# Performance work log

Measured on AMD Instinct MI355X. Metric: run time of the kernel, lower is better.

The kernel has to match this reference:

```python
import jax, jax.numpy as jnp
import numpy as np

B, S, D, H = 2, 2048, 1024, 16
HD = D // H  # 64

def _make_freqs():
    # flux-style rotation matrices: [1,1,S,HD//2,2,2]
    theta = 10000.0
    inv = 1.0 / (theta ** (np.arange(0, HD, 2, dtype=np.float32) / HD))  # [HD//2]
    pos = np.arange(S, dtype=np.float32)
    ang = pos[:, None] * inv[None, :]  # [S, HD//2]
    cos, sin = np.cos(ang), np.sin(ang)
    rot = np.stack([np.stack([cos, -sin], -1), np.stack([sin, cos], -1)], -2)  # [S,HD//2,2,2]
    return jnp.asarray(rot[None, None], dtype=jnp.float32)

def setup_inputs() -> dict:
    key = jax.random.key(0)
    ks = jax.random.split(key, 9)
    sc = 1.0 / np.sqrt(D)
    return {
        "x": jax.random.normal(ks[0], (B, S, D), jnp.float32),
        "freqs": _make_freqs(),
        "Wq": jax.random.normal(ks[1], (D, D), jnp.float32) * sc,
        "bq": jax.random.normal(ks[2], (D,), jnp.float32) * 0.01,
        "Wk": jax.random.normal(ks[3], (D, D), jnp.float32) * sc,
        "bk": jax.random.normal(ks[4], (D,), jnp.float32) * 0.01,
        "Wv": jax.random.normal(ks[5], (D, D), jnp.float32) * sc,
        "bv": jax.random.normal(ks[6], (D,), jnp.float32) * 0.01,
        "Wo": jax.random.normal(ks[7], (D, D), jnp.float32) * sc,
        "bo": jax.random.normal(ks[8], (D,), jnp.float32) * 0.01,
    }

def _apply_rope(xq, xk, freqs):
    # xq/xk: [B,H,S,HD]; freqs: [1,1,S,HD//2,2,2]
    def rot(t):
        t_ = t.reshape(*t.shape[:-1], -1, 1, 2)  # [B,H,S,HD//2,1,2]
        out = freqs[..., 0] * t_[..., 0] + freqs[..., 1] * t_[..., 1]  # [B,H,S,HD//2,2]
        return out.reshape(t.shape).astype(t.dtype)
    return rot(xq), rot(xk)

def reference(x, freqs, Wq, bq, Wk, bk, Wv, bv, Wo, bo):
    b, s, _ = x.shape
    # QKV projections (torch Linear: x @ W.T + b)
    q = (x @ Wq.T + bq).reshape(b, s, H, HD).transpose(0, 2, 1, 3)  # [B,H,S,HD]
    k = (x @ Wk.T + bk).reshape(b, s, H, HD).transpose(0, 2, 1, 3)
    v = (x @ Wv.T + bv).reshape(b, s, H, HD).transpose(0, 2, 1, 3)
    q, k = _apply_rope(q, k, freqs)
    # scaled dot product attention, no mask, no dropout
    scale = 1.0 / jnp.sqrt(jnp.asarray(HD, x.dtype))
    scores = jnp.einsum("bhqd,bhkd->bhqk", q, k) * scale
    attn = jax.nn.softmax(scores, axis=-1)
    o = jnp.einsum("bhqk,bhkd->bhqd", attn, v)  # [B,H,S,HD]
    o = o.transpose(0, 2, 1, 3).reshape(b, s, D)
    return o @ Wo.T + bo
```

## Files before the change

kernel.cpp:

```cpp
#include <hip/hip_runtime.h>
#include <cmath>

#define B_ 2
#define S_ 2048
#define D_ 1024
#define H_ 16
#define HD_ 64
#define M_ 4096

typedef __attribute__((ext_vector_type(8))) short short8;
typedef __attribute__((ext_vector_type(4))) short short4v;
typedef __attribute__((ext_vector_type(4))) float f32x4;

__device__ __forceinline__ short f2bf(float x) {
    unsigned u = __builtin_bit_cast(unsigned, x);
    u += 0x7fffu + ((u >> 16) & 1u);
    return (short)(u >> 16);
}

__device__ __forceinline__ void gload_lds16(const short* g, short* l) {
    __builtin_amdgcn_global_load_lds(
        (const __attribute__((address_space(1))) unsigned int*)g,
        (__attribute__((address_space(3))) unsigned int*)l, 16, 0, 0);
}

__global__ __launch_bounds__(256) void cast_all_kernel(
    const float* __restrict__ x,  const float* __restrict__ Wq,
    const float* __restrict__ Wk, const float* __restrict__ Wv,
    const float* __restrict__ Wo,
    short* __restrict__ xb, short* __restrict__ Wqkvb, short* __restrict__ Wob)
{
    const size_t i = (size_t)blockIdx.x * 256 + threadIdx.x;
    const float* src; short* dst; size_t off;
    if (i < 1048576)      { src = x;  dst = xb;              off = i; }
    else if (i < 1310720) { src = Wq; dst = Wqkvb;           off = i - 1048576; }
    else if (i < 1572864) { src = Wk; dst = Wqkvb + 1048576; off = i - 1310720; }
    else if (i < 1835008) { src = Wv; dst = Wqkvb + 2097152; off = i - 1572864; }
    else                  { src = Wo; dst = Wob;             off = i - 1835008; }
    float4 v = ((const float4*)src)[off];
    short4v o = { f2bf(v.x), f2bf(v.y), f2bf(v.z), f2bf(v.w) };
    ((short4v*)dst)[off] = o;
}

template<int MODE, int TM, int TN>
__global__ __launch_bounds__(256) void gemm_chunk(
    const short* __restrict__ A, const short* __restrict__ Bw,
    const float* __restrict__ b0p, const float* __restrict__ b1p, const float* __restrict__ b2p,
    const float* __restrict__ freqs,
    void* __restrict__ out0, void* __restrict__ out1, void* __restrict__ out2)
{
    constexpr int RT = TM / 32, CT = TN / 32;
    __shared__ __align__(16) short As[4*TM*32];
    __shared__ __align__(16) short Bs[4*TN*32];
    const int t = threadIdx.x;
    const int w = t >> 6;
    const int lane = t & 63;
    const int qd = lane >> 4, l = lane & 15;
    const int n0 = blockIdx.x * TN, m0 = blockIdx.y * TM;
    const int wr = (w >> 1) * (TM/2), wc = (w & 1) * (TN/2);
    const int srow = lane >> 2;
    const int scol = (lane & 3) * 8;

    f32x4 acc[RT][CT] = {};

    for (int k0 = 0; k0 < 1024; k0 += 128) {
        __syncthreads();
        #pragma unroll
        for (int sub = 0; sub < 4; ++sub) {
            #pragma unroll
            for (int j = 0; j < TM/64; ++j) {
                const int rr = (j*4 + w) * 16;
                gload_lds16(A + (size_t)(m0 + rr + srow)*1024 + k0 + sub*32 + scol,
                            &As[sub*TM*32 + rr*32]);
            }
            #pragma unroll
            for (int j = 0; j < TN/64; ++j) {
                const int rr = (j*4 + w) * 16;
                gload_lds16(Bw + (size_t)(n0 + rr + srow)*1024 + k0 + sub*32 + scol,
                            &Bs[sub*TN*32 + rr*32]);
            }
        }
        __syncthreads();
        #pragma unroll
        for (int sub = 0; sub < 4; ++sub) {
            short8 af[RT], bf[CT];
            #pragma unroll
            for (int rt = 0; rt < RT; ++rt)
                af[rt] = *(const short8*)&As[sub*TM*32 + (wr + rt*16 + l)*32 + qd*8];
            #pragma unroll
            for (int ct = 0; ct < CT; ++ct)
                bf[ct] = *(const short8*)&Bs[sub*TN*32 + (wc + ct*16 + l)*32 + qd*8];
            #pragma unroll
            for (int rt = 0; rt < RT; ++rt)
                #pragma unroll
                for (int ct = 0; ct < CT; ++ct)
                    acc[rt][ct] = __builtin_amdgcn_mfma_f32_16x16x32_bf16(af[rt], bf[ct], acc[rt][ct], 0, 0, 0);
        }
    }

    if (MODE == 0) {
        float* out = (float*)out0;
        #pragma unroll
        for (int rt = 0; rt < RT; ++rt)
            #pragma unroll
            for (int ct = 0; ct < CT; ++ct) {
                const int n = n0 + wc + ct*16 + l;
                const float bias = b0p[n];
                #pragma unroll
                for (int r = 0; r < 4; ++r) {
                    const int m = m0 + wr + rt*16 + qd*4 + r;
                    out[(size_t)m*1024 + n] = acc[rt][ct][r] + bias;
                }
            }
    } else {
        const int sel = n0 >> 10;
        const int nb = n0 & 1023;
        const float* bias = (sel == 0) ? b0p : (sel == 1) ? b1p : b2p;
        if (sel < 2) {
            short* outg = (short*)((sel == 0) ? out0 : out1);
            #pragma unroll
            for (int rt = 0; rt < RT; ++rt)
                #pragma unroll
                for (int ct = 0; ct < CT; ++ct) {
                    const int d = nb + wc + ct*16 + l;
                    const float bsv = bias[d];
                    const int h = d >> 6, hd = d & 63;
                    #pragma unroll
                    for (int r = 0; r < 4; ++r) {
                        const int m = m0 + wr + rt*16 + qd*4 + r;
                        const int bb = m >> 11, s = m & 2047;
                        float val = acc[rt][ct][r] + bsv;
                        float pv = __shfl_xor(val, 1);
                        const float* f = freqs + (size_t)s*128 + (size_t)(hd >> 1)*4;
                        float o = (d & 1) ? (f[2]*pv + f[3]*val) : (f[0]*val + f[1]*pv);
                        outg[((size_t)(bb*16 + h)*2048 + s)*64 + hd] = f2bf(o);
                    }
                }
        } else {
            short* outv = (short*)out2;
            #pragma unroll
            for (int rt = 0; rt < RT; ++rt)
                #pragma unroll
                for (int ct = 0; ct < CT; ++ct) {
                    const int d = nb + wc + ct*16 + l;
                    const float bsv = bias[d];
                    const int h = d >> 6, hd = d & 63;
                    const int m0r = m0 + wr + rt*16 + qd*4;
                    const int bb = m0r >> 11, s0 = m0r & 2047;
                    short4v pk;
                    #pragma unroll
                    for (int r = 0; r < 4; ++r) pk[r] = f2bf(acc[rt][ct][r] + bsv);
                    *(short4v*)&outv[((size_t)(bb*16 + h)*64 + hd)*2048 + s0] = pk;
                }
        }
    }
}

__global__ __launch_bounds__(256) void attn_mfma(
    const short* __restrict__ qg, const short* __restrict__ kg,
    const short* __restrict__ vtg, short* __restrict__ og)
{
    __shared__ __align__(16) short Kb[2][64*64];
    __shared__ __align__(16) short Vb[2][64*64];
    __shared__ __align__(16) short Pb[128*64];

    const int t = threadIdx.x;
    const int w = t >> 6;
    const int lane = t & 63;
    const int qd = lane >> 4, l = lane & 15;
    const int l7 = lane & 7;
    const int q0 = blockIdx.x * 128;
    const int bh = blockIdx.y;

    const int rl  = lane >> 3;
    const int ss8 = ((lane & 7) ^ rl) << 3;

    short8 qf[2][2];
    const short* qb = qg + ((size_t)bh*2048 + q0 + w*32)*64;
    #pragma unroll
    for (int rt = 0; rt < 2; ++rt)
        #pragma unroll
        for (int kf = 0; kf < 2; ++kf)
            qf[rt][kf] = *(const short8*)&qb[(rt*16 + l)*64 + kf*32 + qd*8];

    f32x4 oacc[2][4] = {};
    float lsum[2] = {};

    const short* kbase = kg  + (size_t)bh*2048*64;
    const short* vbase = vtg + (size_t)bh*64*2048;
    const float SC = 0.125f * 1.44269504088896340736f;

    {
        gload_lds16(kbase + (size_t)(w*8 + rl)*64 + ss8,        &Kb[0][(w*8)*64]);
        gload_lds16(kbase + (size_t)(32 + w*8 + rl)*64 + ss8,   &Kb[0][(32 + w*8)*64]);
        gload_lds16(vbase + (size_t)(w*8 + rl)*2048 + ss8,      &Vb[0][(w*8)*64]);
        gload_lds16(vbase + (size_t)(32 + w*8 + rl)*2048 + ss8, &Vb[0][(32 + w*8)*64]);
    }
    __syncthreads();

    for (int kt = 0; kt < 32; ++kt) {
        const int buf = kt & 1;

        if (kt + 1 < 32) {
            const short* k2 = kbase + (size_t)(kt + 1)*64*64;
            const short* v2 = vbase + (size_t)(kt + 1)*64;
            gload_lds16(k2 + (size_t)(w*8 + rl)*64 + ss8,        &Kb[buf^1][(w*8)*64]);
            gload_lds16(k2 + (size_t)(32 + w*8 + rl)*64 + ss8,   &Kb[buf^1][(32 + w*8)*64]);
            gload_lds16(v2 + (size_t)(w*8 + rl)*2048 + ss8,      &Vb[buf^1][(w*8)*64]);
            gload_lds16(v2 + (size_t)(32 + w*8 + rl)*2048 + ss8, &Vb[buf^1][(32 + w*8)*64]);
        }

        f32x4 sacc[2][4] = {};
        #pragma unroll
        for (int ct = 0; ct < 4; ++ct) {
            short8 k0f = *(const short8*)&Kb[buf][(ct*16 + l)*64 + (((0 + qd) ^ l7) << 3)];
            short8 k1f = *(const short8*)&Kb[buf][(ct*16 + l)*64 + (((4 + qd) ^ l7) << 3)];
            #pragma unroll
            for (int rt = 0; rt < 2; ++rt) {
                sacc[rt][ct] = __builtin_amdgcn_mfma_f32_16x16x32_bf16(k0f, qf[rt][0], sacc[rt][ct], 0, 0, 0);
                sacc[rt][ct] = __builtin_amdgcn_mfma_f32_16x16x32_bf16(k1f, qf[rt][1], sacc[rt][ct], 0, 0, 0);
            }
        }

        #pragma unroll
        for (int rt = 0; rt < 2; ++rt)
            #pragma unroll
            for (int ct = 0; ct < 4; ++ct) {
                float p0 = exp2f(sacc[rt][ct][0] * SC);
                float p1 = exp2f(sacc[rt][ct][1] * SC);
                float p2 = exp2f(sacc[rt][ct][2] * SC);
                float p3 = exp2f(sacc[rt][ct][3] * SC);
                lsum[rt] += (p0 + p1) + (p2 + p3);
                union { unsigned u[2]; short4v s; } cv;
                asm("v_cvt_pk_bf16_f32 %0, %1, %2" : "=v"(cv.u[0]) : "v"(p0), "v"(p1));
                asm("v_cvt_pk_bf16_f32 %0, %1, %2" : "=v"(cv.u[1]) : "v"(p2), "v"(p3));
                *(short4v*)&Pb[(w*32 + rt*16 + l)*64 + (((ct*32 + qd*8) ^ (l7 << 4)) >> 1)] = cv.s;
            }

        #pragma unroll
        for (int kf = 0; kf < 2; ++kf) {
            const int so = ((kf*4 + qd) ^ l7) << 3;
            short8 pa0 = *(const short8*)&Pb[(w*32 +  0 + l)*64 + so];
            short8 pa1 = *(const short8*)&Pb[(w*32 + 16 + l)*64 + so];
            #pragma unroll
            for (int ht = 0; ht < 4; ++ht) {
                short8 vb = *(const short8*)&Vb[buf][(ht*16 + l)*64 + so];
                oacc[0][ht] = __builtin_amdgcn_mfma_f32_16x16x32_bf16(pa0, vb, oacc[0][ht], 0, 0, 0);
                oacc[1][ht] = __builtin_amdgcn_mfma_f32_16x16x32_bf16(pa1, vb, oacc[1][ht], 0, 0, 0);
            }
        }

        __syncthreads();
    }

    #pragma unroll
    for (int rt = 0; rt < 2; ++rt) {
        lsum[rt] += __shfl_xor(lsum[rt], 16);
        lsum[rt] += __shfl_xor(lsum[rt], 32);
    }
    float inv[2][4];
    #pragma unroll
    for (int rt = 0; rt < 2; ++rt)
        #pragma unroll
        for (int r = 0; r < 4; ++r)
            inv[rt][r] = 1.0f / __shfl(lsum[rt], qd*4 + r);

    const int bb = bh >> 4, h = bh & 15;
    #pragma unroll
    for (int rt = 0; rt < 2; ++rt)
        #pragma unroll
        for (int ht = 0; ht < 4; ++ht)
            #pragma unroll
            for (int r = 0; r < 4; ++r) {
                const int s = q0 + w*32 + rt*16 + qd*4 + r;
                og[((size_t)bb*2048 + s)*1024 + h*64 + ht*16 + l] =
                    f2bf(oacc[rt][ht][r] * inv[rt][r]);
            }
}

extern "C" void kernel_launch(void* const* d_in, const int* in_sizes, int n_in,
                              void* d_out, int out_size, void* d_ws, size_t ws_size,
                              hipStream_t stream)
{
    const float* x  = (const float*)d_in[0];
    const float* fr = (const float*)d_in[1];
    const float* Wq = (const float*)d_in[2];
    const float* bq = (const float*)d_in[3];
    const float* Wk = (const float*)d_in[4];
    const float* bk = (const float*)d_in[5];
    const float* Wv = (const float*)d_in[6];
    const float* bv = (const float*)d_in[7];
    const float* Wo = (const float*)d_in[8];
    const float* bo = (const float*)d_in[9];
    float* out = (float*)d_out;

    short* ws    = (short*)d_ws;
    short* xb    = ws;
    short* Wqkvb = xb    + 4194304;
    short* Wob   = Wqkvb + 3145728;
    short* qg    = Wob   + 1048576;
    short* kg    = qg    + 4194304;
    short* vtg   = kg    + 4194304;
    short* og    = vtg   + 4194304;

    cast_all_kernel<<<8192, 256, 0, stream>>>(x, Wq, Wk, Wv, Wo, xb, Wqkvb, Wob);
    gemm_chunk<1,128,64><<<dim3(48, 32), 256, 0, stream>>>(xb, Wqkvb, bq, bk, bv, fr, qg, kg, vtg);
    attn_mfma<<<dim3(16, 32), 256, 0, stream>>>(qg, kg, vtg, og);
    gemm_chunk<0,64,64><<<dim3(16, 64), 256, 0, stream>>>(og, Wob, bo, nullptr, nullptr, nullptr,
                                                          out, nullptr, nullptr);
}
```

Before: 249.8 us.

## Split attention work across eight waves and retune GEMM tiles and K-chunk depth

The attention kernel now runs 512 threads per block, with each of eight waves owning 16 query rows instead of four waves owning 32. Each wave also loads a single K/V row slice per tile, which roughly halves per-wave registers and spreads tile loads over more waves. The GEMMs gain a template parameter for K-chunk depth, set to 64. The QKV projection tile grows to 128x128 and the output projection tile to 128x64. This trades fewer K-tile rows per sync and less per-wave work for more barriers per K loop and fewer blocks in flight for the GEMMs.

```diff
diff --git a/kernel.cpp b/kernel.cpp
--- a/kernel.cpp
+++ b/kernel.cpp
@@ -42,7 +42,7 @@
     ((short4v*)dst)[off] = o;
 }
 
-template<int MODE, int TM, int TN>
+template<int MODE, int TM, int TN, int NSUB>
 __global__ __launch_bounds__(256) void gemm_chunk(
     const short* __restrict__ A, const short* __restrict__ Bw,
     const float* __restrict__ b0p, const float* __restrict__ b1p, const float* __restrict__ b2p,
@@ -50,8 +50,8 @@
     void* __restrict__ out0, void* __restrict__ out1, void* __restrict__ out2)
 {
     constexpr int RT = TM / 32, CT = TN / 32;
-    __shared__ __align__(16) short As[4*TM*32];
-    __shared__ __align__(16) short Bs[4*TN*32];
+    __shared__ __align__(16) short As[NSUB*TM*32];
+    __shared__ __align__(16) short Bs[NSUB*TN*32];
     const int t = threadIdx.x;
     const int w = t >> 6;
     const int lane = t & 63;
@@ -63,10 +63,10 @@
 
     f32x4 acc[RT][CT] = {};
 
-    for (int k0 = 0; k0 < 1024; k0 += 128) {
+    for (int k0 = 0; k0 < 1024; k0 += NSUB*32) {
         __syncthreads();
         #pragma unroll
-        for (int sub = 0; sub < 4; ++sub) {
+        for (int sub = 0; sub < NSUB; ++sub) {
             #pragma unroll
             for (int j = 0; j < TM/64; ++j) {
                 const int rr = (j*4 + w) * 16;
@@ -82,7 +82,7 @@
         }
         __syncthreads();
         #pragma unroll
-        for (int sub = 0; sub < 4; ++sub) {
+        for (int sub = 0; sub < NSUB; ++sub) {
             short8 af[RT], bf[CT];
             #pragma unroll
             for (int rt = 0; rt < RT; ++rt)
@@ -156,7 +156,7 @@
     }
 }
 
-__global__ __launch_bounds__(256) void attn_mfma(
+__global__ __launch_bounds__(512) void attn_mfma(
     const short* __restrict__ qg, const short* __restrict__ kg,
     const short* __restrict__ vtg, short* __restrict__ og)
 {
@@ -175,107 +175,85 @@
     const int rl  = lane >> 3;
     const int ss8 = ((lane & 7) ^ rl) << 3;
 
-    short8 qf[2][2];
-    const short* qb = qg + ((size_t)bh*2048 + q0 + w*32)*64;
+    short8 qf[2];
+    const short* qb = qg + ((size_t)bh*2048 + q0 + w*16)*64;
     #pragma unroll
-    for (int rt = 0; rt < 2; ++rt)
-        #pragma unroll
-        for (int kf = 0; kf < 2; ++kf)
-            qf[rt][kf] = *(const short8*)&qb[(rt*16 + l)*64 + kf*32 + qd*8];
-
-    f32x4 oacc[2][4] = {};
-    float lsum[2] = {};
+    for (int kf = 0; kf < 2; ++kf)
+        qf[kf] = *(const short8*)&qb[l*64 + kf*32 + qd*8];
+
+    f32x4 oacc[4] = {};
+    float lsum = 0.f;
 
     const short* kbase = kg  + (size_t)bh*2048*64;
     const short* vbase = vtg + (size_t)bh*64*2048;
     const float SC = 0.125f * 1.44269504088896340736f;
 
-    {
-        gload_lds16(kbase + (size_t)(w*8 + rl)*64 + ss8,        &Kb[0][(w*8)*64]);
-        gload_lds16(kbase + (size_t)(32 + w*8 + rl)*64 + ss8,   &Kb[0][(32 + w*8)*64]);
-        gload_lds16(vbase + (size_t)(w*8 + rl)*2048 + ss8,      &Vb[0][(w*8)*64]);
-        gload_lds16(vbase + (size_t)(32 + w*8 + rl)*2048 + ss8, &Vb[0][(32 + w*8)*64]);
-    }
+    gload_lds16(kbase + (size_t)(w*8 + rl)*64 + ss8,   &Kb[0][(w*8)*64]);
+    gload_lds16(vbase + (size_t)(w*8 + rl)*2048 + ss8, &Vb[0][(w*8)*64]);
     __syncthreads();
 
     for (int kt = 0; kt < 32; ++kt) {
         const int buf = kt & 1;
 
         if (kt + 1 < 32) {
-            const short* k2 = kbase + (size_t)(kt + 1)*64*64;
-            const short* v2 = vbase + (size_t)(kt + 1)*64;
-            gload_lds16(k2 + (size_t)(w*8 + rl)*64 + ss8,        &Kb[buf^1][(w*8)*64]);
-            gload_lds16(k2 + (size_t)(32 + w*8 + rl)*64 + ss8,   &Kb[buf^1][(32 + w*8)*64]);
-            gload_lds16(v2 + (size_t)(w*8 + rl)*2048 + ss8,      &Vb[buf^1][(w*8)*64]);
-            gload_lds16(v2 + (size_t)(32 + w*8 + rl)*2048 + ss8, &Vb[buf^1][(32 + w*8)*64]);
-        }
-
-        f32x4 sacc[2][4] = {};
+            gload_lds16(kbase + (size_t)((kt+1)*64 + w*8 + rl)*64 + ss8,
+                        &Kb[buf^1][(w*8)*64]);
+            gload_lds16(vbase + (size_t)(w*8 + rl)*2048 + (kt+1)*64 + ss8,
+                        &Vb[buf^1][(w*8)*64]);
+        }
+
+        f32x4 sacc[4] = {};
         #pragma unroll
         for (int ct = 0; ct < 4; ++ct) {
             short8 k0f = *(const short8*)&Kb[buf][(ct*16 + l)*64 + (((0 + qd) ^ l7) << 3)];
             short8 k1f = *(const short8*)&Kb[buf][(ct*16 + l)*64 + (((4 + qd) ^ l7) << 3)];
-            #pragma unroll
-            for (int rt = 0; rt < 2; ++rt) {
-                sacc[rt][ct] = __builtin_amdgcn_mfma_f32_16x16x32_bf16(k0f, qf[rt][0], sacc[rt][ct], 0, 0, 0);
-                sacc[rt][ct] = __builtin_amdgcn_mfma_f32_16x16x32_bf16(k1f, qf[rt][1], sacc[rt][ct], 0, 0, 0);
-            }
-        }
-
-        #pragma unroll
-        for (int rt = 0; rt < 2; ++rt)
-            #pragma unroll
-            for (int ct = 0; ct < 4; ++ct) {
-                float p0 = exp2f(sacc[rt][ct][0] * SC);
-                float p1 = exp2f(sacc[rt][ct][1] * SC);
-                float p2 = exp2f(sacc[rt][ct][2] * SC);
-                float p3 = exp2f(sacc[rt][ct][3] * SC);
-                lsum[rt] += (p0 + p1) + (p2 + p3);
-                union { unsigned u[2]; short4v s; } cv;
-                asm("v_cvt_pk_bf16_f32 %0, %1, %2" : "=v"(cv.u[0]) : "v"(p0), "v"(p1));
-                asm("v_cvt_pk_bf16_f32 %0, %1, %2" : "=v"(cv.u[1]) : "v"(p2), "v"(p3));
-                *(short4v*)&Pb[(w*32 + rt*16 + l)*64 + (((ct*32 + qd*8) ^ (l7 << 4)) >> 1)] = cv.s;
-            }
+            sacc[ct] = __builtin_amdgcn_mfma_f32_16x16x32_bf16(k0f, qf[0], sacc[ct], 0, 0, 0);
+            sacc[ct] = __builtin_amdgcn_mfma_f32_16x16x32_bf16(k1f, qf[1], sacc[ct], 0, 0, 0);
+        }
+
+        #pragma unroll
+        for (int ct = 0; ct < 4; ++ct) {
+            float p0 = exp2f(sacc[ct][0] * SC);
+            float p1 = exp2f(sacc[ct][1] * SC);
+            float p2 = exp2f(sacc[ct][2] * SC);
+            float p3 = exp2f(sacc[ct][3] * SC);
+            lsum += (p0 + p1) + (p2 + p3);
+            union { unsigned u[2]; short4v s; } cv;
+            asm("v_cvt_pk_bf16_f32 %0, %1, %2" : "=v"(cv.u[0]) : "v"(p0), "v"(p1));
+            asm("v_cvt_pk_bf16_f32 %0, %1, %2" : "=v"(cv.u[1]) : "v"(p2), "v"(p3));
+            *(short4v*)&Pb[(w*16 + l)*64 + (((ct*32 + qd*8) ^ (l7 << 4)) >> 1)] = cv.s;
+        }
 
         #pragma unroll
         for (int kf = 0; kf < 2; ++kf) {
             const int so = ((kf*4 + qd) ^ l7) << 3;
-            short8 pa0 = *(const short8*)&Pb[(w*32 +  0 + l)*64 + so];
-            short8 pa1 = *(const short8*)&Pb[(w*32 + 16 + l)*64 + so];
+            short8 pa = *(const short8*)&Pb[(w*16 + l)*64 + so];
             #pragma unroll
             for (int ht = 0; ht < 4; ++ht) {
                 short8 vb = *(const short8*)&Vb[buf][(ht*16 + l)*64 + so];
-                oacc[0][ht] = __builtin_amdgcn_mfma_f32_16x16x32_bf16(pa0, vb, oacc[0][ht], 0, 0, 0);
-                oacc[1][ht] = __builtin_amdgcn_mfma_f32_16x16x32_bf16(pa1, vb, oacc[1][ht], 0, 0, 0);
+                oacc[ht] = __builtin_amdgcn_mfma_f32_16x16x32_bf16(pa, vb, oacc[ht], 0, 0, 0);
             }
         }
 
         __syncthreads();
     }
 
+    lsum += __shfl_xor(lsum, 16);
+    lsum += __shfl_xor(lsum, 32);
+    float inv[4];
     #pragma unroll
-    for (int rt = 0; rt < 2; ++rt) {
-        lsum[rt] += __shfl_xor(lsum[rt], 16);
-        lsum[rt] += __shfl_xor(lsum[rt], 32);
-    }
-    float inv[2][4];
-    #pragma unroll
-    for (int rt = 0; rt < 2; ++rt)
-        #pragma unroll
-        for (int r = 0; r < 4; ++r)
-            inv[rt][r] = 1.0f / __shfl(lsum[rt], qd*4 + r);
+    for (int r = 0; r < 4; ++r)
+        inv[r] = 1.0f / __shfl(lsum, qd*4 + r);
 
     const int bb = bh >> 4, h = bh & 15;
     #pragma unroll
-    for (int rt = 0; rt < 2; ++rt)
-        #pragma unroll
-        for (int ht = 0; ht < 4; ++ht)
-            #pragma unroll
-            for (int r = 0; r < 4; ++r) {
-                const int s = q0 + w*32 + rt*16 + qd*4 + r;
-                og[((size_t)bb*2048 + s)*1024 + h*64 + ht*16 + l] =
-                    f2bf(oacc[rt][ht][r] * inv[rt][r]);
-            }
+    for (int ht = 0; ht < 4; ++ht)
+        #pragma unroll
+        for (int r = 0; r < 4; ++r) {
+            const int s = q0 + w*16 + qd*4 + r;
+            og[((size_t)bb*2048 + s)*1024 + h*64 + ht*16 + l] =
+                f2bf(oacc[ht][r] * inv[r]);
+        }
 }
 
 extern "C" void kernel_launch(void* const* d_in, const int* in_sizes, int n_in,
@@ -304,8 +282,8 @@
     short* og    = vtg   + 4194304;
 
     cast_all_kernel<<<8192, 256, 0, stream>>>(x, Wq, Wk, Wv, Wo, xb, Wqkvb, Wob);
-    gemm_chunk<1,128,64><<<dim3(48, 32), 256, 0, stream>>>(xb, Wqkvb, bq, bk, bv, fr, qg, kg, vtg);
-    attn_mfma<<<dim3(16, 32), 256, 0, stream>>>(qg, kg, vtg, og);
-    gemm_chunk<0,64,64><<<dim3(16, 64), 256, 0, stream>>>(og, Wob, bo, nullptr, nullptr, nullptr,
-                                                          out, nullptr, nullptr);
-}
+    gemm_chunk<1,128,128,2><<<dim3(24, 32), 256, 0, stream>>>(xb, Wqkvb, bq, bk, bv, fr, qg, kg, vtg);
+    attn_mfma<<<dim3(16, 32), 512, 0, stream>>>(qg, kg, vtg, og);
+    gemm_chunk<0,128,64,2><<<dim3(16, 32), 256, 0, stream>>>(og, Wob, bo, nullptr, nullptr, nullptr,
+                                                             out, nullptr, nullptr);
+}
```

Result: no change. 253.6 us (+1.5%).
